# Kernel tuning notes

Hardware: AMD Instinct MI355X
Metric: run time of the kernel (lower is better)

The kernel has to match this reference:

```python
import jax, jax.numpy as jnp
import numpy as np

ALPHA = 1000.0  # softmin temperature from the original module


def setup_inputs() -> dict:
    key = jax.random.key(0)
    ks = jax.random.split(key, 10)
    B, D, H, E, K = 8192, 784, 256, 32, 512
    s = 0.05  # small init scale to keep activations/distances numerically sane
    return {
        "x": jax.random.normal(ks[0], (B, D), jnp.float32),
        "cluster_reps": jax.random.normal(ks[1], (K, E), jnp.float32),
        "W1": jax.random.normal(ks[2], (D, H), jnp.float32) * s,
        "b1": jnp.zeros((H,), jnp.float32),
        "W2": jax.random.normal(ks[3], (H, E), jnp.float32) * s,
        "b2": jnp.zeros((E,), jnp.float32),
        "W3": jax.random.normal(ks[4], (E, H), jnp.float32) * s,
        "b3": jnp.zeros((H,), jnp.float32),
        "W4": jax.random.normal(ks[5], (H, D), jnp.float32) * s,
        "b4": jnp.zeros((D,), jnp.float32),
    }


def reference(x, cluster_reps, W1, b1, W2, b2, W3, b3, W4, b4):
    # --- autoencoder: 2-layer MLP encoder / decoder ---
    h = jax.nn.relu(x @ W1 + b1)            # [B, H]
    embeddings = h @ W2 + b2                # [B, E]
    h2 = jax.nn.relu(embeddings @ W3 + b3)  # [B, H]
    reconstruction = h2 @ W4 + b4           # [B, D]

    # --- squared distances to cluster reps: [B, K] ---
    diff = embeddings[:, None, :] - cluster_reps[None, :, :]  # [B, K, E]
    distances = jnp.sum(diff * diff, axis=2)                  # [B, K]

    # --- stable softmin-weighted distances ---
    min_dist = jnp.min(distances, axis=1, keepdims=True)       # [B, 1]
    exponentials = jnp.exp(-ALPHA * (distances - min_dist))    # [B, K]
    sum_exponentials = jnp.sum(exponentials, axis=1, keepdims=True)
    weighted_dists = distances * (exponentials / sum_exponentials)

    return (weighted_dists, distances, reconstruction, embeddings)
```

## Files before the change

### kernel.cpp

```cpp
#include <hip/hip_runtime.h>
#include <cstddef>

#define NB 8192
#define ND 784
#define NH 256
#define NE 32
#define NK 512
#define ALPHA_F 1000.0f

typedef _Float16 h8 __attribute__((ext_vector_type(8)));
typedef float f32x4 __attribute__((ext_vector_type(4)));

#define TW1 25
#define TN1 8
#define NBW1 200
#define TW4 8
#define TN4 25
#define NBW4 200
#define NBW2 8
#define NBW3 8

__global__ __launch_bounds__(256)
void prep4_kernel(const float* __restrict__ W1, _Float16* __restrict__ w1thi,
                  _Float16* __restrict__ w1tlo,
                  const float* __restrict__ W4, _Float16* __restrict__ w4thi,
                  _Float16* __restrict__ w4tlo,
                  const float* __restrict__ W2, _Float16* __restrict__ w2thi,
                  _Float16* __restrict__ w2tlo,
                  const float* __restrict__ W3, _Float16* __restrict__ w3thi,
                  _Float16* __restrict__ w3tlo) {
    __shared__ float tile[32][33];
    const int b   = blockIdx.x;
    const int tid = threadIdx.x;

    const float* W; _Float16 *hi, *lo; int K, N, kt, nt;
    if (b < NBW1) {
        W = W1; hi = w1thi; lo = w1tlo; K = ND; N = NH;
        kt = b % TW1; nt = b / TW1;
    } else if (b < NBW1 + NBW4) {
        const int bb = b - NBW1;
        W = W4; hi = w4thi; lo = w4tlo; K = NH; N = ND;
        kt = bb % TW4; nt = bb / TW4;
    } else if (b < NBW1 + NBW4 + NBW2) {
        W = W2; hi = w2thi; lo = w2tlo; K = NH; N = NE;
        kt = b - (NBW1 + NBW4); nt = 0;
    } else {
        W = W3; hi = w3thi; lo = w3tlo; K = NE; N = NH;
        kt = 0; nt = b - (NBW1 + NBW4 + NBW2);
    }
    const int k0 = kt * 32, n0 = nt * 32;
    const int row = tid >> 3, c4 = (tid & 7) * 4;
    #pragma unroll
    for (int j = 0; j < 4; ++j) {
        const int k = k0 + row, n = n0 + c4 + j;
        tile[row][c4 + j] = (k < K && n < N) ? W[(size_t)k * N + n] : 0.f;
    }
    __syncthreads();
    const int n = n0 + row;
    if (n < N) {
        #pragma unroll
        for (int j = 0; j < 4; ++j) {
            const int k = k0 + c4 + j;
            if (k < K) {
                float w = tile[c4 + j][row];
                _Float16 hh = (_Float16)w;
                float r = w - (float)hh;
                hi[(size_t)n * K + k] = hh;
                lo[(size_t)n * K + k] = (_Float16)(r * 2048.0f);
            }
        }
    }
}

__global__ __launch_bounds__(512, 1)
void mega_kernel(const float* __restrict__ x, const float* __restrict__ reps,
                 const _Float16* __restrict__ w1thi, const _Float16* __restrict__ w1tlo,
                 const _Float16* __restrict__ w2thi, const _Float16* __restrict__ w2tlo,
                 const _Float16* __restrict__ w3thi, const _Float16* __restrict__ w3tlo,
                 const _Float16* __restrict__ w4thi, const _Float16* __restrict__ w4tlo,
                 const float* __restrict__ b1, const float* __restrict__ b2,
                 const float* __restrict__ b3, const float* __restrict__ b4,
                 float* __restrict__ emb_g, float* __restrict__ recon_g,
                 float* __restrict__ dist_g, float* __restrict__ wout_g) {
    __shared__ __align__(16) unsigned char lds[135936];
    _Float16* R0h  = (_Float16*)lds;
    _Float16* sA   = (_Float16*)(lds + 81920);
    _Float16* hP   = (_Float16*)(lds + 92160);
    float*    es   = (float*)(lds + 125952);
    _Float16* eP   = (_Float16*)(lds + 130560);
    float*    rmin = (float*)(lds + 135680);
    float*    rinv = (float*)(lds + 135808);

    const int tid  = threadIdx.x;
    const int lane = tid & 63;
    const int wv   = tid >> 6;
    const int li   = lane & 15;
    const int kq   = (lane >> 4) * 8;
    const int quad = lane >> 4;
    const int r0   = blockIdx.x * 32;

    const float c1 = 1.0f / 2048.0f;
    const float c2 = c1 * c1;

    {
        _Float16* sBhi = R0h;
        _Float16* sBlo = R0h + 2 * 256 * 40;
        _Float16* sAhi = sA;
        _Float16* sAlo = sA + 2 * 32 * 40;
        const int arow = (tid & 127) >> 2;
        const int ak   = (tid & 3) * 8;
        const int brow = tid >> 1;
        const int bk   = (tid & 1) * 16;
        const float*    pA  = x + (size_t)(r0 + arow) * ND;
        const _Float16* pBh = w1thi + (size_t)brow * ND;
        const _Float16* pBl = w1tlo + (size_t)brow * ND;

        float araw[8];
        h8 rb0, rb1, rb2, rb3;

        auto pf = [&](int s) {
            if (tid < 128) {
                const int k = s * 32 + ak;
                if (k + 8 <= ND) {
                    f32x4 v0 = *(const f32x4*)(pA + k);
                    f32x4 v1 = *(const f32x4*)(pA + k + 4);
                    #pragma unroll
                    for (int j = 0; j < 4; ++j) {
                        araw[j] = v0[j]; araw[4 + j] = v1[j];
                    }
                } else {
                    #pragma unroll
                    for (int j = 0; j < 8; ++j) araw[j] = 0.f;
                }
            }
            const int kb = s * 32 + bk;
            rb0 = (kb + 8  <= ND) ? *(const h8*)(pBh + kb)     : (h8){};
            rb1 = (kb + 16 <= ND) ? *(const h8*)(pBh + kb + 8) : (h8){};
            rb2 = (kb + 8  <= ND) ? *(const h8*)(pBl + kb)     : (h8){};
            rb3 = (kb + 16 <= ND) ? *(const h8*)(pBl + kb + 8) : (h8){};
        };
        auto cm = [&](int buf) {
            if (tid < 128) {
                h8 hi, lo;
                #pragma unroll
                for (int j = 0; j < 8; ++j) {
                    float v = araw[j];
                    _Float16 hh = (_Float16)v;
                    hi[j] = hh;
                    lo[j] = (_Float16)((v - (float)hh) * 2048.0f);
                }
                *(h8*)&sAhi[buf * 32 * 40 + arow * 40 + ak] = hi;
                *(h8*)&sAlo[buf * 32 * 40 + arow * 40 + ak] = lo;
            }
            *(h8*)&sBhi[buf * 256 * 40 + brow * 40 + bk]     = rb0;
            *(h8*)&sBhi[buf * 256 * 40 + brow * 40 + bk + 8] = rb1;
            *(h8*)&sBlo[buf * 256 * 40 + brow * 40 + bk]     = rb2;
            *(h8*)&sBlo[buf * 256 * 40 + brow * 40 + bk + 8] = rb3;
        };

        pf(0); cm(0); pf(1);
        __syncthreads();

        f32x4 a0[2][2] = {}, a1[2][2] = {}, a2[2][2] = {};
        for (int s = 0; s < 25; ++s) {
            const int buf = s & 1;
            h8 fah[2], fal[2], fbh[2], fbl[2];
            #pragma unroll
            for (int mt = 0; mt < 2; ++mt) {
                const int ao = buf * 32 * 40 + (mt * 16 + li) * 40 + kq;
                fah[mt] = *(const h8*)&sAhi[ao];
                fal[mt] = *(const h8*)&sAlo[ao];
            }
            #pragma unroll
            for (int nt = 0; nt < 2; ++nt) {
                const int bo = buf * 256 * 40 + (wv * 32 + nt * 16 + li) * 40 + kq;
                fbh[nt] = *(const h8*)&sBhi[bo];
                fbl[nt] = *(const h8*)&sBlo[bo];
            }
            #pragma unroll
            for (int mt = 0; mt < 2; ++mt)
                #pragma unroll
                for (int nt = 0; nt < 2; ++nt) {
                    a0[mt][nt] = __builtin_amdgcn_mfma_f32_16x16x32_f16(
                        fah[mt], fbh[nt], a0[mt][nt], 0, 0, 0);
                    a1[mt][nt] = __builtin_amdgcn_mfma_f32_16x16x32_f16(
                        fah[mt], fbl[nt], a1[mt][nt], 0, 0, 0);
                    a1[mt][nt] = __builtin_amdgcn_mfma_f32_16x16x32_f16(
                        fal[mt], fbh[nt], a1[mt][nt], 0, 0, 0);
                    a2[mt][nt] = __builtin_amdgcn_mfma_f32_16x16x32_f16(
                        fal[mt], fbl[nt], a2[mt][nt], 0, 0, 0);
                }
            if (s + 1 < 25) { cm((s + 1) & 1); if (s + 2 < 25) pf(s + 2); }
            __syncthreads();
        }
        _Float16* hhi = hP;
        _Float16* hlo = hP + 32 * 264;
        #pragma unroll
        for (int nt = 0; nt < 2; ++nt) {
            const int n = wv * 32 + nt * 16 + li;
            const float bv = b1[n];
            #pragma unroll
            for (int mt = 0; mt < 2; ++mt)
                #pragma unroll
                for (int r = 0; r < 4; ++r) {
                    const int m = mt * 16 + quad * 4 + r;
                    float v = a0[mt][nt][r] + c1 * a1[mt][nt][r]
                            + c2 * a2[mt][nt][r] + bv;
                    v = fmaxf(v, 0.f);
                    _Float16 hh = (_Float16)v;
                    hhi[m * 264 + n] = hh;
                    hlo[m * 264 + n] = (_Float16)((v - (float)hh) * 2048.0f);
                }
        }
    }
    __syncthreads();

    {
        _Float16* w2h = R0h;
        _Float16* w2l = R0h + 32 * 264;
        #pragma unroll
        for (int i = 0; i < 2; ++i) {
            const int cc  = tid + i * 512;
            const int row = cc >> 5, off = (cc & 31) * 8;
            *(h8*)&w2h[row * 264 + off] = *(const h8*)(w2thi + row * 256 + off);
            *(h8*)&w2l[row * 264 + off] = *(const h8*)(w2tlo + row * 256 + off);
        }
    }
    __syncthreads();
    if (wv < 4) {
        const int mt = wv >> 1, nt = wv & 1;
        _Float16* hhi = hP;
        _Float16* hlo = hP + 32 * 264;
        _Float16* w2h = R0h;
        _Float16* w2l = R0h + 32 * 264;
        f32x4 e0 = {}, e1 = {}, e2 = {};
        #pragma unroll
        for (int ks = 0; ks < 8; ++ks) {
            h8 ah = *(const h8*)&hhi[(mt * 16 + li) * 264 + ks * 32 + kq];
            h8 al = *(const h8*)&hlo[(mt * 16 + li) * 264 + ks * 32 + kq];
            h8 bh = *(const h8*)&w2h[(nt * 16 + li) * 264 + ks * 32 + kq];
            h8 bl = *(const h8*)&w2l[(nt * 16 + li) * 264 + ks * 32 + kq];
            e0 = __builtin_amdgcn_mfma_f32_16x16x32_f16(ah, bh, e0, 0, 0, 0);
            e1 = __builtin_amdgcn_mfma_f32_16x16x32_f16(ah, bl, e1, 0, 0, 0);
            e1 = __builtin_amdgcn_mfma_f32_16x16x32_f16(al, bh, e1, 0, 0, 0);
            e2 = __builtin_amdgcn_mfma_f32_16x16x32_f16(al, bl, e2, 0, 0, 0);
        }
        const int ccol = nt * 16 + li;
        const float bv = b2[ccol];
        _Float16* ehi = eP;
        _Float16* elo = eP + 32 * 40;
        #pragma unroll
        for (int r = 0; r < 4; ++r) {
            const int m = mt * 16 + quad * 4 + r;
            float v = e0[r] + c1 * e1[r] + c2 * e2[r] + bv;
            es[m * 36 + ccol] = v;
            _Float16 hh = (_Float16)v;
            ehi[m * 40 + ccol] = hh;
            elo[m * 40 + ccol] = (_Float16)((v - (float)hh) * 2048.0f);
            emb_g[(size_t)(r0 + m) * NE + ccol] = v;
        }
    }
    __syncthreads();

    {
        _Float16* w3h = R0h;
        _Float16* w3l = R0h + 256 * 40;
        #pragma unroll
        for (int i = 0; i < 2; ++i) {
            const int cc  = tid + i * 512;
            const int row = cc >> 2, off = (cc & 3) * 8;
            *(h8*)&w3h[row * 40 + off] = *(const h8*)(w3thi + row * 32 + off);
            *(h8*)&w3l[row * 40 + off] = *(const h8*)(w3tlo + row * 32 + off);
        }
    }
    __syncthreads();
    {
        const int n0 = wv * 32;
        _Float16* w3h  = R0h;
        _Float16* w3l  = R0h + 256 * 40;
        _Float16* ehi  = eP;
        _Float16* elo  = eP + 32 * 40;
        _Float16* h2hi = hP;
        _Float16* h2lo = hP + 32 * 264;
        h8 ah[2], al[2];
        #pragma unroll
        for (int mt = 0; mt < 2; ++mt) {
            ah[mt] = *(const h8*)&ehi[(mt * 16 + li) * 40 + kq];
            al[mt] = *(const h8*)&elo[(mt * 16 + li) * 40 + kq];
        }
        #pragma unroll
        for (int nt = 0; nt < 2; ++nt) {
            h8 bh = *(const h8*)&w3h[(n0 + nt * 16 + li) * 40 + kq];
            h8 bl = *(const h8*)&w3l[(n0 + nt * 16 + li) * 40 + kq];
            const int col = n0 + nt * 16 + li;
            const float bv = b3[col];
            #pragma unroll
            for (int mt = 0; mt < 2; ++mt) {
                f32x4 q0 = {}, q1 = {}, q2 = {};
                q0 = __builtin_amdgcn_mfma_f32_16x16x32_f16(ah[mt], bh, q0, 0, 0, 0);
                q1 = __builtin_amdgcn_mfma_f32_16x16x32_f16(ah[mt], bl, q1, 0, 0, 0);
                q1 = __builtin_amdgcn_mfma_f32_16x16x32_f16(al[mt], bh, q1, 0, 0, 0);
                q2 = __builtin_amdgcn_mfma_f32_16x16x32_f16(al[mt], bl, q2, 0, 0, 0);
                #pragma unroll
                for (int r = 0; r < 4; ++r) {
                    const int m = mt * 16 + quad * 4 + r;
                    float v = q0[r] + c1 * q1[r] + c2 * q2[r] + bv;
                    v = fmaxf(v, 0.f);
                    _Float16 hh = (_Float16)v;
                    h2hi[m * 264 + col] = hh;
                    h2lo[m * 264 + col] = (_Float16)((v - (float)hh) * 2048.0f);
                }
            }
        }
    }
    __syncthreads();

    {
        _Float16* sBhi = R0h;
        _Float16* sBlo = R0h + 2 * 128 * 40;
        _Float16* h2hi = hP;
        _Float16* h2lo = hP + 32 * 264;
        const int brow = tid >> 2;
        const int bk4  = (tid & 3) * 8;
        h8 rbh, rbl;
        auto pf = [&](int ss) {
            int rg = (ss >> 3) * 128 + brow;
            if (rg > ND - 1) rg = ND - 1;
            const int k = (ss & 7) * 32 + bk4;
            rbh = *(const h8*)(w4thi + (size_t)rg * NH + k);
            rbl = *(const h8*)(w4tlo + (size_t)rg * NH + k);
        };
        auto cm = [&](int ss) {
            const int buf = ss & 1;
            *(h8*)&sBhi[buf * 128 * 40 + brow * 40 + bk4] = rbh;
            *(h8*)&sBlo[buf * 128 * 40 + brow * 40 + bk4] = rbl;
        };
        pf(0); cm(0); pf(1);
        __syncthreads();

        f32x4 q0[2] = {}, q1[2] = {};
        for (int ss = 0; ss < 56; ++ss) {
            const int buf = ss & 1, ks = ss & 7;
            h8 fbh = *(const h8*)&sBhi[buf * 128 * 40 + (wv * 16 + li) * 40 + kq];
            h8 fbl = *(const h8*)&sBlo[buf * 128 * 40 + (wv * 16 + li) * 40 + kq];
            #pragma unroll
            for (int mt = 0; mt < 2; ++mt) {
                h8 ah = *(const h8*)&h2hi[(mt * 16 + li) * 264 + ks * 32 + kq];
                h8 al = *(const h8*)&h2lo[(mt * 16 + li) * 264 + ks * 32 + kq];
                q0[mt] = __builtin_amdgcn_mfma_f32_16x16x32_f16(ah, fbh, q0[mt], 0, 0, 0);
                q1[mt] = __builtin_amdgcn_mfma_f32_16x16x32_f16(ah, fbl, q1[mt], 0, 0, 0);
                q1[mt] = __builtin_amdgcn_mfma_f32_16x16x32_f16(al, fbh, q1[mt], 0, 0, 0);
            }
            if (ss + 1 < 56) { cm(ss + 1); if (ss + 2 < 56) pf(ss + 2); }
            __syncthreads();
            if (ks == 7) {
                const int n = (ss >> 3) * 128 + wv * 16 + li;
                if (n < ND) {
                    const float bv = b4[n];
                    #pragma unroll
                    for (int mt = 0; mt < 2; ++mt)
                        #pragma unroll
                        for (int r = 0; r < 4; ++r) {
                            const int m = mt * 16 + quad * 4 + r;
                            recon_g[(size_t)(r0 + m) * ND + n] =
                                q0[mt][r] + c1 * q1[mt][r] + bv;
                        }
                }
                #pragma unroll
                for (int mt = 0; mt < 2; ++mt) { q0[mt] = {}; q1[mt] = {}; }
            }
        }
    }
    __syncthreads();

    {
        float* tr = (float*)R0h;
        const float* rp = reps + (size_t)tid * NE;
        f32x4 rv[8];
        #pragma unroll
        for (int e4 = 0; e4 < 8; ++e4) rv[e4] = ((const f32x4*)rp)[e4];

        float d[32];
        #pragma unroll
        for (int r = 0; r < 32; ++r) {
            float a = 0.f;
            #pragma unroll
            for (int e4 = 0; e4 < 8; ++e4) {
                f32x4 ev = *(const f32x4*)&es[r * 36 + e4 * 4];
                #pragma unroll
                for (int j = 0; j < 4; ++j) {
                    float t = ev[j] - rv[e4][j];
                    a = fmaf(t, t, a);
                }
            }
            d[r] = a;
            tr[r * 520 + tid] = a;
        }
        __syncthreads();
        #pragma unroll
        for (int p = 0; p < 4; ++p) {
            const int rr = wv * 4 + p;
            f32x4 a = *(const f32x4*)&tr[rr * 520 + lane * 8];
            f32x4 b = *(const f32x4*)&tr[rr * 520 + lane * 8 + 4];
            float m = fminf(fminf(fminf(a[0], a[1]), fminf(a[2], a[3])),
                            fminf(fminf(b[0], b[1]), fminf(b[2], b[3])));
            #pragma unroll
            for (int off = 32; off > 0; off >>= 1)
                m = fminf(m, __shfl_xor(m, off, 64));
            if (lane == 0) rmin[rr] = m;
        }
        __syncthreads();
        float e[32];
        #pragma unroll
        for (int r = 0; r < 32; ++r) {
            e[r] = expf(-ALPHA_F * (d[r] - rmin[r]));
            tr[r * 520 + tid] = e[r];
        }
        __syncthreads();
        #pragma unroll
        for (int p = 0; p < 4; ++p) {
            const int rr = wv * 4 + p;
            f32x4 a = *(const f32x4*)&tr[rr * 520 + lane * 8];
            f32x4 b = *(const f32x4*)&tr[rr * 520 + lane * 8 + 4];
            float s = ((a[0] + a[1]) + (a[2] + a[3])) +
                      ((b[0] + b[1]) + (b[2] + b[3]));
            #pragma unroll
            for (int off = 32; off > 0; off >>= 1)
                s += __shfl_xor(s, off, 64);
            if (lane == 0) rinv[rr] = 1.0f / s;
        }
        __syncthreads();
        #pragma unroll
        for (int r = 0; r < 32; ++r) {
            const size_t row = (size_t)(r0 + r);
            dist_g[row * NK + tid] = d[r];
            wout_g[row * NK + tid] = d[r] * (e[r] * rinv[r]);
        }
    }
}

__global__ __launch_bounds__(256)
void splitw2_kernel(const float* __restrict__ W1, _Float16* __restrict__ w1thi,
                    _Float16* __restrict__ w1tlo,
                    const float* __restrict__ W4, _Float16* __restrict__ w4thi,
                    _Float16* __restrict__ w4tlo) {
    const int b = blockIdx.x;
    const float* W; _Float16 *hi, *lo; int K, N, n;
    if (b < NH) { W = W1; hi = w1thi; lo = w1tlo; K = ND; N = NH; n = b; }
    else        { W = W4; hi = w4thi; lo = w4tlo; K = NH; N = ND; n = b - NH; }
    for (int k = threadIdx.x; k < K; k += 256) {
        float w = W[(size_t)k * N + n];
        _Float16 hh = (_Float16)w;
        float r = w - (float)hh;
        hi[(size_t)n * K + k] = hh;
        lo[(size_t)n * K + k] = (_Float16)(r * 2048.0f);
    }
}

template<int TERMS, bool RELU, bool SPLITA, int MT>
__global__ __launch_bounds__(256)
void mfma_gemm3(const float* __restrict__ Af32,
                const _Float16* __restrict__ Ahi_g,
                const _Float16* __restrict__ Alo_g,
                const _Float16* __restrict__ WThi,
                const _Float16* __restrict__ WTlo,
                const float* __restrict__ bias, float* __restrict__ C,
                int N, int K, int KS) {
    constexpr int BM  = MT * 32;
    constexpr int ACH = BM / 64;
    constexpr int AS  = BM * 40;
    constexpr int BS  = 64 * 40;
    __shared__ __align__(16) _Float16 smem[2 * BM * 40 * 2 + 2 * 64 * 40 * 2];
    _Float16* sAhi = smem;
    _Float16* sAlo = sAhi + 2 * BM * 40;
    _Float16* sBhi = sAlo + 2 * BM * 40;
    _Float16* sBlo = sBhi + 2 * 64 * 40;

    const int tid = threadIdx.x;
    const int bm  = blockIdx.x * BM;
    const int bn  = blockIdx.y * 64;

    const int arow = (ACH == 1) ? (tid >> 2) : (tid >> 1);
    const int ak   = (ACH == 1) ? ((tid & 3) * 8) : ((tid & 1) * 16);
    const int brow = tid >> 2;
    const int bk   = (tid & 3) * 8;

    const float*    pA32 = SPLITA ? Af32 + (size_t)(bm + arow) * K : nullptr;
    const _Float16* pAhi = SPLITA ? nullptr : Ahi_g + (size_t)(bm + arow) * K;
    const _Float16* pAlo = SPLITA ? nullptr : Alo_g + (size_t)(bm + arow) * K;
    int brow_g = bn + brow; if (brow_g > N - 1) brow_g = N - 1;
    const _Float16* pBhi = WThi + (size_t)brow_g * K;
    const _Float16* pBlo = WTlo + (size_t)brow_g * K;

    float araw[ACH * 8];
    h8 rahi[ACH], ralo[ACH];
    h8 rbhi, rblo;

    auto prefetch = [&](int s) {
        #pragma unroll
        for (int c = 0; c < ACH; ++c) {
            const int k = s * 32 + ak + c * 8;
            if (SPLITA) {
                if (k + 8 <= K) {
                    f32x4 v0 = *(const f32x4*)(pA32 + k);
                    f32x4 v1 = *(const f32x4*)(pA32 + k + 4);
                    #pragma unroll
                    for (int j = 0; j < 4; ++j) {
                        araw[c * 8 + j]     = v0[j];
                        araw[c * 8 + 4 + j] = v1[j];
                    }
                } else {
                    #pragma unroll
                    for (int j = 0; j < 8; ++j) araw[c * 8 + j] = 0.f;
                }
            } else {
                rahi[c] = (k + 8 <= K) ? *(const h8*)(pAhi + k) : (h8){};
                ralo[c] = (k + 8 <= K) ? *(const h8*)(pAlo + k) : (h8){};
            }
        }
        const int kb = s * 32 + bk;
        rbhi = (kb + 8 <= K) ? *(const h8*)(pBhi + kb) : (h8){};
        rblo = (kb + 8 <= K) ? *(const h8*)(pBlo + kb) : (h8){};
    };

    auto commit = [&](int buf) {
        #pragma unroll
        for (int c = 0; c < ACH; ++c) {
            h8 hi, lo;
            if (SPLITA) {
                #pragma unroll
                for (int j = 0; j < 8; ++j) {
                    float v = araw[c * 8 + j];
                    _Float16 hh = (_Float16)v;
                    hi[j] = hh;
                    lo[j] = (_Float16)((v - (float)hh) * 2048.0f);
                }
            } else { hi = rahi[c]; lo = ralo[c]; }
            *(h8*)&sAhi[buf * AS + arow * 40 + ak + c * 8] = hi;
            *(h8*)&sAlo[buf * AS + arow * 40 + ak + c * 8] = lo;
        }
        *(h8*)&sBhi[buf * BS + brow * 40 + bk] = rbhi;
        *(h8*)&sBlo[buf * BS + brow * 40 + bk] = rblo;
    };

    prefetch(0);
    commit(0);
    prefetch(1);
    __syncthreads();

    const int lane = tid & 63;
    const int wv   = tid >> 6;
    const int wm   = (wv >> 1) * (MT * 16);
    const int wn   = (wv & 1) * 32;
    const int li   = lane & 15;
    const int kq   = (lane >> 4) * 8;

    f32x4 acc0[MT][2] = {};
    f32x4 acc1[MT][2] = {};
    f32x4 acc2[MT][2] = {};

    for (int s = 0; s < KS; ++s) {
        const int buf = s & 1;
        h8 fahi[MT], falo[MT], fbhi[2], fblo[2];
        #pragma unroll
        for (int mt = 0; mt < MT; ++mt) {
            const int ao = buf * AS + (wm + mt * 16 + li) * 40 + kq;
            fahi[mt] = *(const h8*)&sAhi[ao];
            falo[mt] = *(const h8*)&sAlo[ao];
        }
        #pragma unroll
        for (int nt = 0; nt < 2; ++nt) {
            const int bo = buf * BS + (wn + nt * 16 + li) * 40 + kq;
            fbhi[nt] = *(const h8*)&sBhi[bo];
            fblo[nt] = *(const h8*)&sBlo[bo];
        }
        #pragma unroll
        for (int mt = 0; mt < MT; ++mt)
            #pragma unroll
            for (int nt = 0; nt < 2; ++nt) {
                acc0[mt][nt] = __builtin_amdgcn_mfma_f32_16x16x32_f16(
                    fahi[mt], fbhi[nt], acc0[mt][nt], 0, 0, 0);
                acc1[mt][nt] = __builtin_amdgcn_mfma_f32_16x16x32_f16(
                    fahi[mt], fblo[nt], acc1[mt][nt], 0, 0, 0);
                acc1[mt][nt] = __builtin_amdgcn_mfma_f32_16x16x32_f16(
                    falo[mt], fbhi[nt], acc1[mt][nt], 0, 0, 0);
                if (TERMS == 4)
                    acc2[mt][nt] = __builtin_amdgcn_mfma_f32_16x16x32_f16(
                        falo[mt], fblo[nt], acc2[mt][nt], 0, 0, 0);
            }
        if (s + 1 < KS) {
            commit((s + 1) & 1);
            if (s + 2 < KS) prefetch(s + 2);
        }
        __syncthreads();
    }

    const float c1 = 1.0f / 2048.0f;
    const float c2 = c1 * c1;
    const int quad = lane >> 4;
    #pragma unroll
    for (int nt = 0; nt < 2; ++nt) {
        const int n = bn + wn + nt * 16 + li;
        if (n < N) {
            const float bv = bias[n];
            #pragma unroll
            for (int mt = 0; mt < MT; ++mt) {
                #pragma unroll
                for (int r = 0; r < 4; ++r) {
                    const int m = bm + wm + mt * 16 + quad * 4 + r;
                    float v = acc0[mt][nt][r] + c1 * acc1[mt][nt][r];
                    if (TERMS == 4) v += c2 * acc2[mt][nt][r];
                    v += bv;
                    if (RELU) v = fmaxf(v, 0.f);
                    C[(size_t)m * N + n] = v;
                }
            }
        }
    }
}

__global__ __launch_bounds__(256)
void mid_kernel(const float* __restrict__ h, const float* __restrict__ W2,
                const float* __restrict__ b2, const float* __restrict__ W3,
                const float* __restrict__ b3, float* __restrict__ emb,
                _Float16* __restrict__ h2hi, _Float16* __restrict__ h2lo) {
    __shared__ float es[16][32];
    const int tid = threadIdx.x;
    const int r0  = blockIdx.x * 16;

    #pragma unroll
    for (int half = 0; half < 2; ++half) {
        const int o   = tid + half * 256;
        const int row = o >> 5;
        const int col = o & 31;
        const float* hrow = h + (size_t)(r0 + row) * NH;
        float acc0 = 0.f, acc1 = 0.f;
        #pragma unroll 4
        for (int k = 0; k < NH; k += 4) {
            float4 hv = *(const float4*)(hrow + k);
            acc0 = fmaf(hv.x, W2[(k + 0) * NE + col], acc0);
            acc1 = fmaf(hv.y, W2[(k + 1) * NE + col], acc1);
            acc0 = fmaf(hv.z, W2[(k + 2) * NE + col], acc0);
            acc1 = fmaf(hv.w, W2[(k + 3) * NE + col], acc1);
        }
        float v = acc0 + acc1 + b2[col];
        es[row][col] = v;
        emb[(size_t)r0 * NE + o] = v;
    }
    __syncthreads();

    const int col = tid;
    float acc[16];
    #pragma unroll
    for (int r = 0; r < 16; ++r) acc[r] = 0.f;
    #pragma unroll
    for (int k = 0; k < NE; ++k) {
        float w = W3[k * NH + col];
        #pragma unroll
        for (int r = 0; r < 16; ++r) acc[r] = fmaf(es[r][k], w, acc[r]);
    }
    const float bb = b3[col];
    #pragma unroll
    for (int r = 0; r < 16; ++r) {
        float v = acc[r] + bb;
        v = v > 0.f ? v : 0.f;
        _Float16 hh = (_Float16)v;
        float rr = v - (float)hh;
        h2hi[(size_t)(r0 + r) * NH + col] = hh;
        h2lo[(size_t)(r0 + r) * NH + col] = (_Float16)(rr * 2048.0f);
    }
}

__global__ __launch_bounds__(512, 4)
void dist_kernel(const float* __restrict__ emb, const float* __restrict__ reps,
                 float* __restrict__ dist, float* __restrict__ wout) {
    __shared__ float es[8][32];
    __shared__ float tr[8][520];
    __shared__ float rmin[8];
    __shared__ float rinv[8];

    const int tid = threadIdx.x;
    const int r0  = blockIdx.x * 8;

    if (tid < 256) es[tid >> 5][tid & 31] = emb[(size_t)r0 * NE + tid];

    const float* rp = reps + (size_t)tid * NE;
    f32x4 rv[8];
    #pragma unroll
    for (int e4 = 0; e4 < 8; ++e4) rv[e4] = ((const f32x4*)rp)[e4];
    __syncthreads();

    float d[8];
    #pragma unroll
    for (int r = 0; r < 8; ++r) {
        float a = 0.f;
        #pragma unroll
        for (int e4 = 0; e4 < 8; ++e4) {
            f32x4 ev = *(const f32x4*)&es[r][e4 * 4];
            #pragma unroll
            for (int j = 0; j < 4; ++j) {
                float t = ev[j] - rv[e4][j];
                a = fmaf(t, t, a);
            }
        }
        d[r] = a;
    }

    const int lane = tid & 63;
    const int wv   = tid >> 6;

    #pragma unroll
    for (int r = 0; r < 8; ++r) tr[r][tid] = d[r];
    __syncthreads();
    {
        f32x4 a = *(const f32x4*)&tr[wv][lane * 8];
        f32x4 b = *(const f32x4*)&tr[wv][lane * 8 + 4];
        float m = fminf(fminf(fminf(a[0], a[1]), fminf(a[2], a[3])),
                        fminf(fminf(b[0], b[1]), fminf(b[2], b[3])));
        #pragma unroll
        for (int off = 32; off > 0; off >>= 1)
            m = fminf(m, __shfl_xor(m, off, 64));
        if (lane == 0) rmin[wv] = m;
    }
    __syncthreads();

    float e[8];
    #pragma unroll
    for (int r = 0; r < 8; ++r) {
        e[r] = expf(-ALPHA_F * (d[r] - rmin[r]));
        tr[r][tid] = e[r];
    }
    __syncthreads();
    {
        f32x4 a = *(const f32x4*)&tr[wv][lane * 8];
        f32x4 b = *(const f32x4*)&tr[wv][lane * 8 + 4];
        float s = ((a[0] + a[1]) + (a[2] + a[3])) +
                  ((b[0] + b[1]) + (b[2] + b[3]));
        #pragma unroll
        for (int off = 32; off > 0; off >>= 1)
            s += __shfl_xor(s, off, 64);
        if (lane == 0) rinv[wv] = 1.0f / s;
    }
    __syncthreads();

    #pragma unroll
    for (int r = 0; r < 8; ++r) {
        const size_t row = (size_t)(r0 + r);
        dist[row * NK + tid] = d[r];
        wout[row * NK + tid] = d[r] * (e[r] * rinv[r]);
    }
}

extern "C" void kernel_launch(void* const* d_in, const int* in_sizes, int n_in,
                              void* d_out, int out_size, void* d_ws, size_t ws_size,
                              hipStream_t stream) {
    const float* x    = (const float*)d_in[0];
    const float* reps = (const float*)d_in[1];
    const float* W1   = (const float*)d_in[2];
    const float* b1   = (const float*)d_in[3];
    const float* W2   = (const float*)d_in[4];
    const float* b2   = (const float*)d_in[5];
    const float* W3   = (const float*)d_in[6];
    const float* b3   = (const float*)d_in[7];
    const float* W4   = (const float*)d_in[8];
    const float* b4   = (const float*)d_in[9];

    float* out   = (float*)d_out;
    float* wout  = out;
    float* dist  = out + (size_t)NB * NK;
    float* recon = out + (size_t)2 * NB * NK;
    float* emb   = out + (size_t)2 * NB * NK + (size_t)NB * ND;

    const size_t nW14 = (size_t)ND * NH;
    const size_t nW23 = (size_t)NE * NH;
    const size_t wneed = (4 * nW14 + 4 * nW23) * sizeof(_Float16);

    if (d_ws != nullptr && ws_size >= wneed) {
        _Float16* w1thi = (_Float16*)d_ws;
        _Float16* w1tlo = w1thi + nW14;
        _Float16* w4thi = w1tlo + nW14;
        _Float16* w4tlo = w4thi + nW14;
        _Float16* w2thi = w4tlo + nW14;
        _Float16* w2tlo = w2thi + nW23;
        _Float16* w3thi = w2tlo + nW23;
        _Float16* w3tlo = w3thi + nW23;

        prep4_kernel<<<NBW1 + NBW4 + NBW2 + NBW3, 256, 0, stream>>>(
            W1, w1thi, w1tlo, W4, w4thi, w4tlo,
            W2, w2thi, w2tlo, W3, w3thi, w3tlo);

        mega_kernel<<<NB / 32, 512, 0, stream>>>(
            x, reps, w1thi, w1tlo, w2thi, w2tlo, w3thi, w3tlo, w4thi, w4tlo,
            b1, b2, b3, b4, emb, recon, dist, wout);
    } else {
        float* h = dist;
        _Float16* h2hi  = (_Float16*)(dist + (size_t)NB * NH);
        _Float16* h2lo  = h2hi + (size_t)NB * NH;
        _Float16* w1thi = (_Float16*)wout;
        _Float16* w1tlo = w1thi + (size_t)NH * ND;
        _Float16* w4thi = w1tlo + (size_t)NH * ND;
        _Float16* w4tlo = w4thi + (size_t)ND * NH;

        splitw2_kernel<<<NH + ND, 256, 0, stream>>>(W1, w1thi, w1tlo,
                                                    W4, w4thi, w4tlo);
        mfma_gemm3<4, true, true, 2><<<dim3(128, 4), 256, 0, stream>>>(
            x, nullptr, nullptr, w1thi, w1tlo, b1, h, NH, ND, 25);
        mid_kernel<<<NB / 16, 256, 0, stream>>>(h, W2, b2, W3, b3,
                                                emb, h2hi, h2lo);
        mfma_gemm3<3, false, false, 4><<<dim3(64, 13), 256, 0, stream>>>(
            nullptr, h2hi, h2lo, w4thi, w4tlo, b4, recon, ND, NH, 8);
        dist_kernel<<<NB / 8, 512, 0, stream>>>(emb, reps, dist, wout);
    }
}
```

Baseline: 166.1 us.

## Shrink mega kernel row tile to 16 and stream weights from global into registers

The fused autoencoder kernel now processes 16 rows per block instead of 32 and launches twice as many blocks. Shared memory drops from about 136KB to about 73KB, and the launch bound is raised to allow more resident blocks. The whole x tile is converted to hi/lo fp16 in LDS once, and weight fragments for all four GEMMs are loaded straight from global/L2 into registers with software double-buffering, which removes the per-k-step LDS staging and barriers. The trade-off is that each block re-reads all the weights for only 16 rows, doubling total weight traffic through L2, and each MFMA now covers a single M-tile with less reuse.

```diff
diff --git a/kernel.cpp b/kernel.cpp
--- a/kernel.cpp
+++ b/kernel.cpp
@@ -72,7 +72,10 @@
     }
 }
 
-__global__ __launch_bounds__(512, 1)
+#define XSTR 792
+#define HSTR 264
+
+__global__ __launch_bounds__(512, 4)
 void mega_kernel(const float* __restrict__ x, const float* __restrict__ reps,
                  const _Float16* __restrict__ w1thi, const _Float16* __restrict__ w1tlo,
                  const _Float16* __restrict__ w2thi, const _Float16* __restrict__ w2tlo,
@@ -82,14 +85,19 @@
                  const float* __restrict__ b3, const float* __restrict__ b4,
                  float* __restrict__ emb_g, float* __restrict__ recon_g,
                  float* __restrict__ dist_g, float* __restrict__ wout_g) {
-    __shared__ __align__(16) unsigned char lds[135936];
-    _Float16* R0h  = (_Float16*)lds;
-    _Float16* sA   = (_Float16*)(lds + 81920);
-    _Float16* hP   = (_Float16*)(lds + 92160);
-    float*    es   = (float*)(lds + 125952);
-    _Float16* eP   = (_Float16*)(lds + 130560);
-    float*    rmin = (float*)(lds + 135680);
-    float*    rinv = (float*)(lds + 135808);
+    __shared__ __align__(16) unsigned char lds[72576];
+    _Float16* xh   = (_Float16*)(lds + 0);
+    _Float16* xl   = (_Float16*)(lds + 25344);
+    _Float16* h2h  = (_Float16*)(lds + 0);
+    _Float16* h2l  = (_Float16*)(lds + 8448);
+    float*    tr   = (float*)(lds + 16896);
+    _Float16* hh_  = (_Float16*)(lds + 50688);
+    _Float16* hl_  = (_Float16*)(lds + 59136);
+    float*    es   = (float*)(lds + 67584);
+    _Float16* eh   = (_Float16*)(lds + 69888);
+    _Float16* el   = (_Float16*)(lds + 71168);
+    float*    rmin = (float*)(lds + 72448);
+    float*    rinv = (float*)(lds + 72512);
 
     const int tid  = threadIdx.x;
     const int lane = tid & 63;
@@ -97,292 +105,193 @@
     const int li   = lane & 15;
     const int kq   = (lane >> 4) * 8;
     const int quad = lane >> 4;
-    const int r0   = blockIdx.x * 32;
+    const int r0   = blockIdx.x * 16;
 
     const float c1 = 1.0f / 2048.0f;
     const float c2 = c1 * c1;
 
+    for (int cc = tid; cc < 16 * 98; cc += 512) {
+        const int row = cc / 98;
+        const int col = (cc - row * 98) * 8;
+        const float* p = x + (size_t)(r0 + row) * ND + col;
+        f32x4 v0 = *(const f32x4*)p;
+        f32x4 v1 = *(const f32x4*)(p + 4);
+        h8 hi, lo;
+        #pragma unroll
+        for (int j = 0; j < 4; ++j) {
+            _Float16 a = (_Float16)v0[j];
+            hi[j] = a; lo[j] = (_Float16)((v0[j] - (float)a) * 2048.0f);
+            _Float16 b = (_Float16)v1[j];
+            hi[4 + j] = b; lo[4 + j] = (_Float16)((v1[j] - (float)b) * 2048.0f);
+        }
+        *(h8*)&xh[row * XSTR + col] = hi;
+        *(h8*)&xl[row * XSTR + col] = lo;
+    }
+    __syncthreads();
+
     {
-        _Float16* sBhi = R0h;
-        _Float16* sBlo = R0h + 2 * 256 * 40;
-        _Float16* sAhi = sA;
-        _Float16* sAlo = sA + 2 * 32 * 40;
-        const int arow = (tid & 127) >> 2;
-        const int ak   = (tid & 3) * 8;
-        const int brow = tid >> 1;
-        const int bk   = (tid & 1) * 16;
-        const float*    pA  = x + (size_t)(r0 + arow) * ND;
-        const _Float16* pBh = w1thi + (size_t)brow * ND;
-        const _Float16* pBl = w1tlo + (size_t)brow * ND;
-
-        float araw[8];
-        h8 rb0, rb1, rb2, rb3;
-
-        auto pf = [&](int s) {
-            if (tid < 128) {
-                const int k = s * 32 + ak;
-                if (k + 8 <= ND) {
-                    f32x4 v0 = *(const f32x4*)(pA + k);
-                    f32x4 v1 = *(const f32x4*)(pA + k + 4);
-                    #pragma unroll
-                    for (int j = 0; j < 4; ++j) {
-                        araw[j] = v0[j]; araw[4 + j] = v1[j];
-                    }
-                } else {
-                    #pragma unroll
-                    for (int j = 0; j < 8; ++j) araw[j] = 0.f;
-                }
-            }
-            const int kb = s * 32 + bk;
-            rb0 = (kb + 8  <= ND) ? *(const h8*)(pBh + kb)     : (h8){};
-            rb1 = (kb + 16 <= ND) ? *(const h8*)(pBh + kb + 8) : (h8){};
-            rb2 = (kb + 8  <= ND) ? *(const h8*)(pBl + kb)     : (h8){};
-            rb3 = (kb + 16 <= ND) ? *(const h8*)(pBl + kb + 8) : (h8){};
+        const int nb0 = wv * 32;
+        const _Float16* pB0h = w1thi + (size_t)(nb0 + li) * ND;
+        const _Float16* pB1h = w1thi + (size_t)(nb0 + 16 + li) * ND;
+        const _Float16* pB0l = w1tlo + (size_t)(nb0 + li) * ND;
+        const _Float16* pB1l = w1tlo + (size_t)(nb0 + 16 + li) * ND;
+
+        h8 pb[2][4];
+        auto ldb = [&](int s, int buf) {
+            const int k = s * 32 + kq;
+            const bool ok = (k + 8 <= ND);
+            pb[buf][0] = ok ? *(const h8*)(pB0h + k) : (h8){};
+            pb[buf][1] = ok ? *(const h8*)(pB1h + k) : (h8){};
+            pb[buf][2] = ok ? *(const h8*)(pB0l + k) : (h8){};
+            pb[buf][3] = ok ? *(const h8*)(pB1l + k) : (h8){};
         };
-        auto cm = [&](int buf) {
-            if (tid < 128) {
-                h8 hi, lo;
-                #pragma unroll
-                for (int j = 0; j < 8; ++j) {
-                    float v = araw[j];
-                    _Float16 hh = (_Float16)v;
-                    hi[j] = hh;
-                    lo[j] = (_Float16)((v - (float)hh) * 2048.0f);
-                }
-                *(h8*)&sAhi[buf * 32 * 40 + arow * 40 + ak] = hi;
-                *(h8*)&sAlo[buf * 32 * 40 + arow * 40 + ak] = lo;
-            }
-            *(h8*)&sBhi[buf * 256 * 40 + brow * 40 + bk]     = rb0;
-            *(h8*)&sBhi[buf * 256 * 40 + brow * 40 + bk + 8] = rb1;
-            *(h8*)&sBlo[buf * 256 * 40 + brow * 40 + bk]     = rb2;
-            *(h8*)&sBlo[buf * 256 * 40 + brow * 40 + bk + 8] = rb3;
-        };
-
-        pf(0); cm(0); pf(1);
-        __syncthreads();
-
-        f32x4 a0[2][2] = {}, a1[2][2] = {}, a2[2][2] = {};
-        for (int s = 0; s < 25; ++s) {
+        ldb(0, 0); ldb(1, 1);
+
+        f32x4 a0[2] = {}, a1[2] = {}, a2[2] = {};
+        for (int s = 0; s < 24; ++s) {
             const int buf = s & 1;
-            h8 fah[2], fal[2], fbh[2], fbl[2];
-            #pragma unroll
-            for (int mt = 0; mt < 2; ++mt) {
-                const int ao = buf * 32 * 40 + (mt * 16 + li) * 40 + kq;
-                fah[mt] = *(const h8*)&sAhi[ao];
-                fal[mt] = *(const h8*)&sAlo[ao];
-            }
+            const int k = s * 32 + kq;
+            h8 ah = *(const h8*)&xh[li * XSTR + k];
+            h8 al = *(const h8*)&xl[li * XSTR + k];
             #pragma unroll
             for (int nt = 0; nt < 2; ++nt) {
-                const int bo = buf * 256 * 40 + (wv * 32 + nt * 16 + li) * 40 + kq;
-                fbh[nt] = *(const h8*)&sBhi[bo];
-                fbl[nt] = *(const h8*)&sBlo[bo];
-            }
-            #pragma unroll
-            for (int mt = 0; mt < 2; ++mt)
-                #pragma unroll
-                for (int nt = 0; nt < 2; ++nt) {
-                    a0[mt][nt] = __builtin_amdgcn_mfma_f32_16x16x32_f16(
-                        fah[mt], fbh[nt], a0[mt][nt], 0, 0, 0);
-                    a1[mt][nt] = __builtin_amdgcn_mfma_f32_16x16x32_f16(
-                        fah[mt], fbl[nt], a1[mt][nt], 0, 0, 0);
-                    a1[mt][nt] = __builtin_amdgcn_mfma_f32_16x16x32_f16(
-                        fal[mt], fbh[nt], a1[mt][nt], 0, 0, 0);
-                    a2[mt][nt] = __builtin_amdgcn_mfma_f32_16x16x32_f16(
-                        fal[mt], fbl[nt], a2[mt][nt], 0, 0, 0);
-                }
-            if (s + 1 < 25) { cm((s + 1) & 1); if (s + 2 < 25) pf(s + 2); }
-            __syncthreads();
-        }
-        _Float16* hhi = hP;
-        _Float16* hlo = hP + 32 * 264;
+                a0[nt] = __builtin_amdgcn_mfma_f32_16x16x32_f16(ah, pb[buf][nt],     a0[nt], 0, 0, 0);
+                a1[nt] = __builtin_amdgcn_mfma_f32_16x16x32_f16(ah, pb[buf][2 + nt], a1[nt], 0, 0, 0);
+                a1[nt] = __builtin_amdgcn_mfma_f32_16x16x32_f16(al, pb[buf][nt],     a1[nt], 0, 0, 0);
+                a2[nt] = __builtin_amdgcn_mfma_f32_16x16x32_f16(al, pb[buf][2 + nt], a2[nt], 0, 0, 0);
+            }
+            if (s + 2 <= 24) ldb(s + 2, buf);
+        }
+        {
+            const int k = 768 + kq;
+            h8 ah = {}, al = {};
+            if (k + 8 <= ND) {
+                ah = *(const h8*)&xh[li * XSTR + k];
+                al = *(const h8*)&xl[li * XSTR + k];
+            }
+            #pragma unroll
+            for (int nt = 0; nt < 2; ++nt) {
+                a0[nt] = __builtin_amdgcn_mfma_f32_16x16x32_f16(ah, pb[0][nt],     a0[nt], 0, 0, 0);
+                a1[nt] = __builtin_amdgcn_mfma_f32_16x16x32_f16(ah, pb[0][2 + nt], a1[nt], 0, 0, 0);
+                a1[nt] = __builtin_amdgcn_mfma_f32_16x16x32_f16(al, pb[0][nt],     a1[nt], 0, 0, 0);
+                a2[nt] = __builtin_amdgcn_mfma_f32_16x16x32_f16(al, pb[0][2 + nt], a2[nt], 0, 0, 0);
+            }
+        }
         #pragma unroll
         for (int nt = 0; nt < 2; ++nt) {
-            const int n = wv * 32 + nt * 16 + li;
+            const int n = nb0 + nt * 16 + li;
             const float bv = b1[n];
             #pragma unroll
-            for (int mt = 0; mt < 2; ++mt)
-                #pragma unroll
-                for (int r = 0; r < 4; ++r) {
-                    const int m = mt * 16 + quad * 4 + r;
-                    float v = a0[mt][nt][r] + c1 * a1[mt][nt][r]
-                            + c2 * a2[mt][nt][r] + bv;
-                    v = fmaxf(v, 0.f);
-                    _Float16 hh = (_Float16)v;
-                    hhi[m * 264 + n] = hh;
-                    hlo[m * 264 + n] = (_Float16)((v - (float)hh) * 2048.0f);
-                }
-        }
-    }
-    __syncthreads();
-
-    {
-        _Float16* w2h = R0h;
-        _Float16* w2l = R0h + 32 * 264;
-        #pragma unroll
-        for (int i = 0; i < 2; ++i) {
-            const int cc  = tid + i * 512;
-            const int row = cc >> 5, off = (cc & 31) * 8;
-            *(h8*)&w2h[row * 264 + off] = *(const h8*)(w2thi + row * 256 + off);
-            *(h8*)&w2l[row * 264 + off] = *(const h8*)(w2tlo + row * 256 + off);
-        }
-    }
-    __syncthreads();
-    if (wv < 4) {
-        const int mt = wv >> 1, nt = wv & 1;
-        _Float16* hhi = hP;
-        _Float16* hlo = hP + 32 * 264;
-        _Float16* w2h = R0h;
-        _Float16* w2l = R0h + 32 * 264;
+            for (int r = 0; r < 4; ++r) {
+                const int m = quad * 4 + r;
+                float v = a0[nt][r] + c1 * a1[nt][r] + c2 * a2[nt][r] + bv;
+                v = fmaxf(v, 0.f);
+                _Float16 t = (_Float16)v;
+                hh_[m * HSTR + n] = t;
+                hl_[m * HSTR + n] = (_Float16)((v - (float)t) * 2048.0f);
+            }
+        }
+    }
+    __syncthreads();
+
+    if (wv < 2) {
+        const _Float16* pbh = w2thi + (size_t)(wv * 16 + li) * NH;
+        const _Float16* pbl = w2tlo + (size_t)(wv * 16 + li) * NH;
         f32x4 e0 = {}, e1 = {}, e2 = {};
         #pragma unroll
         for (int ks = 0; ks < 8; ++ks) {
-            h8 ah = *(const h8*)&hhi[(mt * 16 + li) * 264 + ks * 32 + kq];
-            h8 al = *(const h8*)&hlo[(mt * 16 + li) * 264 + ks * 32 + kq];
-            h8 bh = *(const h8*)&w2h[(nt * 16 + li) * 264 + ks * 32 + kq];
-            h8 bl = *(const h8*)&w2l[(nt * 16 + li) * 264 + ks * 32 + kq];
+            const int k = ks * 32 + kq;
+            h8 ah = *(const h8*)&hh_[li * HSTR + k];
+            h8 al = *(const h8*)&hl_[li * HSTR + k];
+            h8 bh = *(const h8*)(pbh + k);
+            h8 bl = *(const h8*)(pbl + k);
             e0 = __builtin_amdgcn_mfma_f32_16x16x32_f16(ah, bh, e0, 0, 0, 0);
             e1 = __builtin_amdgcn_mfma_f32_16x16x32_f16(ah, bl, e1, 0, 0, 0);
             e1 = __builtin_amdgcn_mfma_f32_16x16x32_f16(al, bh, e1, 0, 0, 0);
             e2 = __builtin_amdgcn_mfma_f32_16x16x32_f16(al, bl, e2, 0, 0, 0);
         }
-        const int ccol = nt * 16 + li;
-        const float bv = b2[ccol];
-        _Float16* ehi = eP;
-        _Float16* elo = eP + 32 * 40;
+        const int col = wv * 16 + li;
+        const float bv = b2[col];
         #pragma unroll
         for (int r = 0; r < 4; ++r) {
-            const int m = mt * 16 + quad * 4 + r;
+            const int m = quad * 4 + r;
             float v = e0[r] + c1 * e1[r] + c2 * e2[r] + bv;
-            es[m * 36 + ccol] = v;
-            _Float16 hh = (_Float16)v;
-            ehi[m * 40 + ccol] = hh;
-            elo[m * 40 + ccol] = (_Float16)((v - (float)hh) * 2048.0f);
-            emb_g[(size_t)(r0 + m) * NE + ccol] = v;
+            es[m * 36 + col] = v;
+            _Float16 t = (_Float16)v;
+            eh[m * 40 + col] = t;
+            el[m * 40 + col] = (_Float16)((v - (float)t) * 2048.0f);
+            emb_g[(size_t)(r0 + m) * NE + col] = v;
         }
     }
     __syncthreads();
 
     {
-        _Float16* w3h = R0h;
-        _Float16* w3l = R0h + 256 * 40;
-        #pragma unroll
-        for (int i = 0; i < 2; ++i) {
-            const int cc  = tid + i * 512;
-            const int row = cc >> 2, off = (cc & 3) * 8;
-            *(h8*)&w3h[row * 40 + off] = *(const h8*)(w3thi + row * 32 + off);
-            *(h8*)&w3l[row * 40 + off] = *(const h8*)(w3tlo + row * 32 + off);
-        }
-    }
-    __syncthreads();
+        h8 ah = *(const h8*)&eh[li * 40 + kq];
+        h8 al = *(const h8*)&el[li * 40 + kq];
+        #pragma unroll
+        for (int nt = 0; nt < 2; ++nt) {
+            const int col = wv * 32 + nt * 16 + li;
+            h8 bh = *(const h8*)(w3thi + (size_t)col * NE + kq);
+            h8 bl = *(const h8*)(w3tlo + (size_t)col * NE + kq);
+            f32x4 q0 = {}, q1 = {}, q2 = {};
+            q0 = __builtin_amdgcn_mfma_f32_16x16x32_f16(ah, bh, q0, 0, 0, 0);
+            q1 = __builtin_amdgcn_mfma_f32_16x16x32_f16(ah, bl, q1, 0, 0, 0);
+            q1 = __builtin_amdgcn_mfma_f32_16x16x32_f16(al, bh, q1, 0, 0, 0);
+            q2 = __builtin_amdgcn_mfma_f32_16x16x32_f16(al, bl, q2, 0, 0, 0);
+            const float bv = b3[col];
+            #pragma unroll
+            for (int r = 0; r < 4; ++r) {
+                const int m = quad * 4 + r;
+                float v = q0[r] + c1 * q1[r] + c2 * q2[r] + bv;
+                v = fmaxf(v, 0.f);
+                _Float16 t = (_Float16)v;
+                h2h[m * HSTR + col] = t;
+                h2l[m * HSTR + col] = (_Float16)((v - (float)t) * 2048.0f);
+            }
+        }
+    }
+    __syncthreads();
+
+    for (int p = 0; p < 7; ++p) {
+        const int nbase = p * 128 + wv * 16;
+        if (nbase >= ND) break;
+        const int n = nbase + li;
+        const _Float16* pbh = w4thi + (size_t)n * NH;
+        const _Float16* pbl = w4tlo + (size_t)n * NH;
+        h8 rb[2][2];
+        rb[0][0] = *(const h8*)(pbh + kq);      rb[0][1] = *(const h8*)(pbl + kq);
+        rb[1][0] = *(const h8*)(pbh + 32 + kq); rb[1][1] = *(const h8*)(pbl + 32 + kq);
+        f32x4 q0 = {}, q1 = {};
+        #pragma unroll
+        for (int ks = 0; ks < 8; ++ks) {
+            const int buf = ks & 1;
+            const int k = ks * 32 + kq;
+            h8 ah = *(const h8*)&h2h[li * HSTR + k];
+            h8 al = *(const h8*)&h2l[li * HSTR + k];
+            q0 = __builtin_amdgcn_mfma_f32_16x16x32_f16(ah, rb[buf][0], q0, 0, 0, 0);
+            q1 = __builtin_amdgcn_mfma_f32_16x16x32_f16(ah, rb[buf][1], q1, 0, 0, 0);
+            q1 = __builtin_amdgcn_mfma_f32_16x16x32_f16(al, rb[buf][0], q1, 0, 0, 0);
+            if (ks + 2 < 8) {
+                const int k2 = (ks + 2) * 32 + kq;
+                rb[buf][0] = *(const h8*)(pbh + k2);
+                rb[buf][1] = *(const h8*)(pbl + k2);
+            }
+        }
+        const float bv = b4[n];
+        #pragma unroll
+        for (int r = 0; r < 4; ++r)
+            recon_g[(size_t)(r0 + quad * 4 + r) * ND + n] = q0[r] + c1 * q1[r] + bv;
+    }
+
     {
-        const int n0 = wv * 32;
-        _Float16* w3h  = R0h;
-        _Float16* w3l  = R0h + 256 * 40;
-        _Float16* ehi  = eP;
-        _Float16* elo  = eP + 32 * 40;
-        _Float16* h2hi = hP;
-        _Float16* h2lo = hP + 32 * 264;
-        h8 ah[2], al[2];
-        #pragma unroll
-        for (int mt = 0; mt < 2; ++mt) {
-            ah[mt] = *(const h8*)&ehi[(mt * 16 + li) * 40 + kq];
-            al[mt] = *(const h8*)&elo[(mt * 16 + li) * 40 + kq];
-        }
-        #pragma unroll
-        for (int nt = 0; nt < 2; ++nt) {
-            h8 bh = *(const h8*)&w3h[(n0 + nt * 16 + li) * 40 + kq];
-            h8 bl = *(const h8*)&w3l[(n0 + nt * 16 + li) * 40 + kq];
-            const int col = n0 + nt * 16 + li;
-            const float bv = b3[col];
-            #pragma unroll
-            for (int mt = 0; mt < 2; ++mt) {
-                f32x4 q0 = {}, q1 = {}, q2 = {};
-                q0 = __builtin_amdgcn_mfma_f32_16x16x32_f16(ah[mt], bh, q0, 0, 0, 0);
-                q1 = __builtin_amdgcn_mfma_f32_16x16x32_f16(ah[mt], bl, q1, 0, 0, 0);
-                q1 = __builtin_amdgcn_mfma_f32_16x16x32_f16(al[mt], bh, q1, 0, 0, 0);
-                q2 = __builtin_amdgcn_mfma_f32_16x16x32_f16(al[mt], bl, q2, 0, 0, 0);
-                #pragma unroll
-                for (int r = 0; r < 4; ++r) {
-                    const int m = mt * 16 + quad * 4 + r;
-                    float v = q0[r] + c1 * q1[r] + c2 * q2[r] + bv;
-                    v = fmaxf(v, 0.f);
-                    _Float16 hh = (_Float16)v;
-                    h2hi[m * 264 + col] = hh;
-                    h2lo[m * 264 + col] = (_Float16)((v - (float)hh) * 2048.0f);
-                }
-            }
-        }
-    }
-    __syncthreads();
-
-    {
-        _Float16* sBhi = R0h;
-        _Float16* sBlo = R0h + 2 * 128 * 40;
-        _Float16* h2hi = hP;
-        _Float16* h2lo = hP + 32 * 264;
-        const int brow = tid >> 2;
-        const int bk4  = (tid & 3) * 8;
-        h8 rbh, rbl;
-        auto pf = [&](int ss) {
-            int rg = (ss >> 3) * 128 + brow;
-            if (rg > ND - 1) rg = ND - 1;
-            const int k = (ss & 7) * 32 + bk4;
-            rbh = *(const h8*)(w4thi + (size_t)rg * NH + k);
-            rbl = *(const h8*)(w4tlo + (size_t)rg * NH + k);
-        };
-        auto cm = [&](int ss) {
-            const int buf = ss & 1;
-            *(h8*)&sBhi[buf * 128 * 40 + brow * 40 + bk4] = rbh;
-            *(h8*)&sBlo[buf * 128 * 40 + brow * 40 + bk4] = rbl;
-        };
-        pf(0); cm(0); pf(1);
-        __syncthreads();
-
-        f32x4 q0[2] = {}, q1[2] = {};
-        for (int ss = 0; ss < 56; ++ss) {
-            const int buf = ss & 1, ks = ss & 7;
-            h8 fbh = *(const h8*)&sBhi[buf * 128 * 40 + (wv * 16 + li) * 40 + kq];
-            h8 fbl = *(const h8*)&sBlo[buf * 128 * 40 + (wv * 16 + li) * 40 + kq];
-            #pragma unroll
-            for (int mt = 0; mt < 2; ++mt) {
-                h8 ah = *(const h8*)&h2hi[(mt * 16 + li) * 264 + ks * 32 + kq];
-                h8 al = *(const h8*)&h2lo[(mt * 16 + li) * 264 + ks * 32 + kq];
-                q0[mt] = __builtin_amdgcn_mfma_f32_16x16x32_f16(ah, fbh, q0[mt], 0, 0, 0);
-                q1[mt] = __builtin_amdgcn_mfma_f32_16x16x32_f16(ah, fbl, q1[mt], 0, 0, 0);
-                q1[mt] = __builtin_amdgcn_mfma_f32_16x16x32_f16(al, fbh, q1[mt], 0, 0, 0);
-            }
-            if (ss + 1 < 56) { cm(ss + 1); if (ss + 2 < 56) pf(ss + 2); }
-            __syncthreads();
-            if (ks == 7) {
-                const int n = (ss >> 3) * 128 + wv * 16 + li;
-                if (n < ND) {
-                    const float bv = b4[n];
-                    #pragma unroll
-                    for (int mt = 0; mt < 2; ++mt)
-                        #pragma unroll
-                        for (int r = 0; r < 4; ++r) {
-                            const int m = mt * 16 + quad * 4 + r;
-                            recon_g[(size_t)(r0 + m) * ND + n] =
-                                q0[mt][r] + c1 * q1[mt][r] + bv;
-                        }
-                }
-                #pragma unroll
-                for (int mt = 0; mt < 2; ++mt) { q0[mt] = {}; q1[mt] = {}; }
-            }
-        }
-    }
-    __syncthreads();
-
-    {
-        float* tr = (float*)R0h;
         const float* rp = reps + (size_t)tid * NE;
         f32x4 rv[8];
         #pragma unroll
         for (int e4 = 0; e4 < 8; ++e4) rv[e4] = ((const f32x4*)rp)[e4];
 
-        float d[32];
-        #pragma unroll
-        for (int r = 0; r < 32; ++r) {
+        float d[16];
+        #pragma unroll
+        for (int r = 0; r < 16; ++r) {
             float a = 0.f;
             #pragma unroll
             for (int e4 = 0; e4 < 8; ++e4) {
@@ -398,32 +307,32 @@
         }
         __syncthreads();
         #pragma unroll
-        for (int p = 0; p < 4; ++p) {
-            const int rr = wv * 4 + p;
-            f32x4 a = *(const f32x4*)&tr[rr * 520 + lane * 8];
-            f32x4 b = *(const f32x4*)&tr[rr * 520 + lane * 8 + 4];
-            float m = fminf(fminf(fminf(a[0], a[1]), fminf(a[2], a[3])),
-                            fminf(fminf(b[0], b[1]), fminf(b[2], b[3])));
+        for (int p = 0; p < 2; ++p) {
+            const int rr = wv * 2 + p;
+            float m = tr[rr * 520 + lane];
+            #pragma unroll
+            for (int j = 1; j < 8; ++j)
+                m = fminf(m, tr[rr * 520 + lane + 64 * j]);
             #pragma unroll
             for (int off = 32; off > 0; off >>= 1)
                 m = fminf(m, __shfl_xor(m, off, 64));
             if (lane == 0) rmin[rr] = m;
         }
         __syncthreads();
-        float e[32];
-        #pragma unroll
-        for (int r = 0; r < 32; ++r) {
+        float e[16];
+        #pragma unroll
+        for (int r = 0; r < 16; ++r) {
             e[r] = expf(-ALPHA_F * (d[r] - rmin[r]));
             tr[r * 520 + tid] = e[r];
         }
         __syncthreads();
         #pragma unroll
-        for (int p = 0; p < 4; ++p) {
-            const int rr = wv * 4 + p;
-            f32x4 a = *(const f32x4*)&tr[rr * 520 + lane * 8];
-            f32x4 b = *(const f32x4*)&tr[rr * 520 + lane * 8 + 4];
-            float s = ((a[0] + a[1]) + (a[2] + a[3])) +
-                      ((b[0] + b[1]) + (b[2] + b[3]));
+        for (int p = 0; p < 2; ++p) {
+            const int rr = wv * 2 + p;
+            float s = tr[rr * 520 + lane];
+            #pragma unroll
+            for (int j = 1; j < 8; ++j)
+                s += tr[rr * 520 + lane + 64 * j];
             #pragma unroll
             for (int off = 32; off > 0; off >>= 1)
                 s += __shfl_xor(s, off, 64);
@@ -431,7 +340,7 @@
         }
         __syncthreads();
         #pragma unroll
-        for (int r = 0; r < 32; ++r) {
+        for (int r = 0; r < 16; ++r) {
             const size_t row = (size_t)(r0 + r);
             dist_g[row * NK + tid] = d[r];
             wout_g[row * NK + tid] = d[r] * (e[r] * rinv[r]);
@@ -789,7 +698,7 @@
             W1, w1thi, w1tlo, W4, w4thi, w4tlo,
             W2, w2thi, w2tlo, W3, w3thi, w3tlo);
 
-        mega_kernel<<<NB / 32, 512, 0, stream>>>(
+        mega_kernel<<<NB / 16, 512, 0, stream>>>(
             x, reps, w1thi, w1tlo, w2thi, w2tlo, w3thi, w3tlo, w4thi, w4tlo,
             b1, b2, b3, b4, emb, recon, dist, wout);
     } else {
```

Result: slower. 185.4 us (+11.6%).
